# Kernel tuning notes

Hardware: AMD Instinct MI355X
Metric: run time of the kernel (lower is better)

## Reference

```python
import jax, jax.numpy as jnp
import numpy as np

Lx, Ly, D, P = 4, 5, 4, 2
DEPTH = 5
TAU = 0.1
N = Lx * Ly
B = 64


def setup_inputs() -> dict:
    key = jax.random.key(0)
    k1, k2, k3 = jax.random.split(key, 3)
    # PEPS site tensors: [Lx, Ly, phys, up, down, left, right]; boundary bonds sliced to dim 1 at use.
    peps = jax.random.normal(k1, (Lx, Ly, P, D, D, D, D), dtype=jnp.float32) * 0.5
    # Two-site Trotter gate: expm(-tau * h) for a random symmetric two-body term h (4x4).
    h = jax.random.normal(k2, (4, 4), dtype=jnp.float32)
    h = 0.5 * (h + h.T)
    w, v = jnp.linalg.eigh(h)
    gate = (v * jnp.exp(-TAU * w)) @ v.T  # [4,4]
    x = jax.random.randint(k3, (B, N), 0, 2, dtype=jnp.int32)
    return {"x": x, "peps": peps, "gate": gate}


def _slice_boundary(site, i, j):
    # site: [p, u, d, l, r]; open boundary -> bond dim 1 on lattice edges
    if i == 0:
        site = site[:, :1]
    if i == Lx - 1:
        site = site[:, :, :1]
    if j == 0:
        site = site[:, :, :, :1]
    if j == Ly - 1:
        site = site[..., :1]
    return site


def _peps_statevector(peps):
    # Exact contraction of the open-boundary PEPS to the full 2^N statevector.
    rows = []
    for i in range(Lx):
        T = jnp.ones((1, 1, 1, 1), dtype=peps.dtype)  # [Pphys, Uup, Ddown, l]
        for j in range(Ly):
            s = _slice_boundary(peps[i, j], i, j)
            T = jnp.einsum('PUDl,pudlr->PpUuDdr', T, s)
            Pn, p, U, u, Dn, d, r = T.shape
            T = T.reshape(Pn * p, U * u, Dn * d, r)
        rows.append(T[..., 0])  # [2^Ly, up_bonds, down_bonds]
    S = jnp.ones((1, 1), dtype=peps.dtype)  # [Pphys, down_bonds]
    for row in rows:
        S = jnp.einsum('PU,QUD->PQD', S, row)
        a, b, c = S.shape
        S = S.reshape(a * b, c)
    return S[:, 0]  # [2^N]


def _apply_gate(psi, g, a, b):
    # g: [2,2,2,2] = gate[o1,o2,i1,i2]; psi: (2,)*N
    out = jnp.tensordot(g, psi, axes=([2, 3], [a, b]))
    return jnp.moveaxis(out, (0, 1), (a, b))


def _bonds():
    horiz = [((i, j), (i, j + 1)) for i in range(Lx) for j in range(Ly - 1)]
    vert = [((i, j), (i + 1, j)) for i in range(Lx - 1) for j in range(Ly)]
    return horiz + vert


def reference(x, peps, gate):
    psi = _peps_statevector(peps).reshape((2,) * N)
    g = gate.reshape(2, 2, 2, 2)
    bonds = _bonds()
    for _ in range(DEPTH):
        for (i1, j1), (i2, j2) in bonds:
            psi = _apply_gate(psi, g, i1 * Ly + j1, i2 * Ly + j2)
    psi = psi.reshape(-1)
    pw = 2 ** jnp.arange(N - 1, -1, -1, dtype=jnp.int32)
    idx = (x * pw).sum(axis=1)
    return psi[idx]  # [B] amplitudes
```

## Files before the change

kernel.cpp:

```cpp
#include <hip/hip_runtime.h>


#define PAD(i) ((i) + (((i) >> 4) << 2))
#define PIDX(i,j,p,u,d,l,r) (((((((i)*5+(j))*2+(p))*4+(u))*4+(d))*4+(l))*4+(r))

static constexpr int COL0  = 0;
static constexpr int COL1  = 4096;
static constexpr int COL2  = COL1 + 1048576;
static constexpr int COL3  = COL2 + 1048576;
static constexpr int COL4  = COL3 + 1048576;
static constexpr int M01TO = COL4 + 4096;
static constexpr int M34TO = M01TO + 65536;
static constexpr int T12TO = M34TO + 65536;
static constexpr int PSIO  = T12TO + 1048576;

__global__ __launch_bounds__(256) void k_build_cols(const float* __restrict__ peps,
                                                    float* __restrict__ ws) {
  __shared__ float p01[4096], p23[4096];
  int bid = blockIdx.x, t = threadIdx.x;
  if (bid < 384) {
    int col = 1 + (bid >> 7);
    int part = bid & 127;
#pragma unroll
    for (int k = 0; k < 16; ++k) {
      int e = k * 256 + t;
      int r12 = e & 15, l12 = (e >> 4) & 15, d2 = (e >> 8) & 3, p = e >> 10;
      int l1 = l12 >> 2, l2 = l12 & 3, r1 = r12 >> 2, r2 = r12 & 3;
      float s01 = 0.f, s23 = 0.f;
#pragma unroll
      for (int d = 0; d < 4; ++d) {
        s01 += peps[PIDX(0, col, (p >> 1), 0, d, l1, r1)] *
               peps[PIDX(1, col, (p & 1), d, d2, l2, r2)];
        s23 += peps[PIDX(2, col, (p >> 1), d2, d, l1, r1)] *
               peps[PIDX(3, col, (p & 1), d, 0, l2, r2)];
      }
      p01[e] = s01;
      p23[e] = s23;
    }
    __syncthreads();
    const int coloffs[3] = {COL1, COL2, COL3};
    float* out = ws + coloffs[col - 1];
#pragma unroll
    for (int k = 0; k < 8; ++k) {
      int eq = part * 8192 + (k * 256 + t) * 4;
      int r34b = eq & 15;
      int r12 = (eq >> 4) & 15, l34 = (eq >> 8) & 15, l12 = (eq >> 12) & 15;
      int p = eq >> 16;
      int pa = p >> 2, pb = p & 3;
      float4 acc = {0.f, 0.f, 0.f, 0.f};
#pragma unroll
      for (int d2 = 0; d2 < 4; ++d2) {
        float a01 = p01[((((pa * 4 + d2) << 4) | l12) << 4) | r12];
        const float4 b4 =
            *(const float4*)&p23[((((pb * 4 + d2) << 4) | l34) << 4) | r34b];
        acc.x += a01 * b4.x;
        acc.y += a01 * b4.y;
        acc.z += a01 * b4.z;
        acc.w += a01 * b4.w;
      }
      *(float4*)&out[eq] = acc;
    }
  } else {
    int col = (bid == 384) ? 0 : 4;
    const int lsh = (col == 0) ? 0 : 2;
    const int rsh = (col == 4) ? 0 : 2;
    const int ldim = 1 << lsh, rdim = 1 << rsh;
    const int LLB = 2 * lsh, RRB = 2 * rsh;
    const int LL = 1 << LLB, RR = 1 << RRB;
    int n12 = (LL * RR) << 4;
    for (int e = t; e < n12; e += 256) {
      int r12 = e & (RR - 1);
      int l12 = (e >> RRB) & (LL - 1);
      int d2 = (e >> (RRB + LLB)) & 3;
      int p = e >> (RRB + LLB + 2);
      int l1 = l12 >> lsh, l2 = l12 & (ldim - 1);
      int r1 = r12 >> rsh, r2 = r12 & (rdim - 1);
      float s01 = 0.f, s23 = 0.f;
      for (int d = 0; d < 4; ++d) {
        s01 += peps[PIDX(0, col, (p >> 1), 0, d, l1, r1)] *
               peps[PIDX(1, col, (p & 1), d, d2, l2, r2)];
        s23 += peps[PIDX(2, col, (p >> 1), d2, d, l1, r1)] *
               peps[PIDX(3, col, (p & 1), d, 0, l2, r2)];
      }
      p01[e] = s01;
      p23[e] = s23;
    }
    __syncthreads();
    const int LB = 2 * LLB, RB = 2 * RRB;
    int total = 16 << (LB + RB);
    float* out = ws + ((col == 0) ? COL0 : COL4);
    for (int e = t; e < total; e += 256) {
      int r = e & ((1 << RB) - 1);
      int l = (e >> RB) & ((1 << LB) - 1);
      int p = e >> (RB + LB);
      int r34 = r & (RR - 1), r12 = r >> RRB;
      int l34 = l & (LL - 1), l12 = l >> LLB;
      int pa = p >> 2, pb = p & 3;
      float s = 0.f;
      for (int d2 = 0; d2 < 4; ++d2) {
        s += p01[((((pa * 4 + d2) << LLB) | l12) << RRB) | r12] *
             p23[((((pb * 4 + d2) << LLB) | l34) << RRB) | r34];
      }
      out[e] = s;
    }
  }
}

__global__ __launch_bounds__(256) void k_small(const float* __restrict__ ws,
                                               float* __restrict__ m01,
                                               float* __restrict__ m34t) {
  __shared__ float c3buf[4112], c4buf[4112];
  int t = threadIdx.x;
  if (blockIdx.x < 64) {
    int c1 = blockIdx.x >> 2, q = blockIdx.x & 3;
    int r2l = t & 63, c0g = t >> 6;
    int R2 = q * 64 + r2l;
    const float* col0 = ws + COL0;
    const float* col1 = ws + COL1;
    float a0 = 0.f, a1 = 0.f, a2 = 0.f, a3 = 0.f;
    for (int R1 = 0; R1 < 256; ++R1) {
      float bv = col1[(c1 * 256 + R1) * 256 + R2];
      a0 += col0[(c0g * 4 + 0) * 256 + R1] * bv;
      a1 += col0[(c0g * 4 + 1) * 256 + R1] * bv;
      a2 += col0[(c0g * 4 + 2) * 256 + R1] * bv;
      a3 += col0[(c0g * 4 + 3) * 256 + R1] * bv;
    }
    m01[((c0g * 4 + 0) * 16 + c1) * 256 + R2] = a0;
    m01[((c0g * 4 + 1) * 16 + c1) * 256 + R2] = a1;
    m01[((c0g * 4 + 2) * 16 + c1) * 256 + R2] = a2;
    m01[((c0g * 4 + 3) * 16 + c1) * 256 + R2] = a3;
  } else {
    int L3 = blockIdx.x - 64;
    const float* col3 = ws + COL3;
    const float* col4 = ws + COL4;
    for (int e = t; e < 4096; e += 256) {
      c4buf[(e >> 8) * 257 + (e & 255)] = col4[e];
      c3buf[(e >> 8) * 257 + (e & 255)] =
          col3[(e >> 8) * 65536 + L3 * 256 + (e & 255)];
    }
    __syncthreads();
    int c3 = t >> 4, c4 = t & 15;
    float acc = 0.f;
    for (int B = 0; B < 256; ++B)
      acc += c3buf[c3 * 257 + B] * c4buf[c4 * 257 + B];
    m34t[L3 * 256 + t] = acc;
  }
}

__global__ __launch_bounds__(256) void k_t012(const float* __restrict__ m01,
                                              const float* __restrict__ col2,
                                              float* __restrict__ t012) {
  __shared__ float A[4096];
  int t = threadIdx.x;
  int c2 = blockIdx.x & 15, tg = blockIdx.x >> 4;
#pragma unroll
  for (int k = 0; k < 4; ++k)
    *(float4*)&A[(k * 256 + t) * 4] =
        *(const float4*)&m01[tg * 4096 + (k * 256 + t) * 4];
  __syncthreads();
  float acc[16] = {};
  for (int R2 = 0; R2 < 256; R2 += 4) {
    float b0 = col2[c2 * 65536 + (R2 + 0) * 256 + t];
    float b1 = col2[c2 * 65536 + (R2 + 1) * 256 + t];
    float b2 = col2[c2 * 65536 + (R2 + 2) * 256 + t];
    float b3 = col2[c2 * 65536 + (R2 + 3) * 256 + t];
#pragma unroll
    for (int i = 0; i < 16; ++i) {
      float4 a4 = *(const float4*)&A[i * 256 + R2];
      acc[i] += a4.x * b0 + a4.y * b1 + a4.z * b2 + a4.w * b3;
    }
  }
#pragma unroll
  for (int i = 0; i < 16; ++i)
    t012[c2 * 65536 + (tg * 16 + i) * 256 + t] = acc[i];
}

__global__ __launch_bounds__(256) void k_psi0(const float* __restrict__ t012,
                                              const float* __restrict__ m34t,
                                              float* __restrict__ psi) {
  __shared__ float A[4096];
  int t = threadIdx.x;
  int tg = blockIdx.x;
#pragma unroll
  for (int i = 0; i < 16; ++i)
    A[i * 256 + t] = t012[i * 65536 + tg * 256 + t];
  __syncthreads();
  float acc[16] = {};
  for (int L3 = 0; L3 < 256; L3 += 4) {
    float b0 = m34t[(L3 + 0) * 256 + t];
    float b1 = m34t[(L3 + 1) * 256 + t];
    float b2 = m34t[(L3 + 2) * 256 + t];
    float b3 = m34t[(L3 + 3) * 256 + t];
#pragma unroll
    for (int i = 0; i < 16; ++i) {
      float4 a4 = *(const float4*)&A[i * 256 + L3];
      acc[i] += a4.x * b0 + a4.y * b1 + a4.z * b2 + a4.w * b3;
    }
  }
#pragma unroll
  for (int i = 0; i < 16; ++i)
    psi[(tg * 16 + i) * 256 + t] = acc[i];
}

template <int NB, int HI, int LO>
__device__ __forceinline__ void gate2(float* x, const float* __restrict__ g) {
  constexpr int H = 1 << HI, L = 1 << LO, N = 1 << NB;
#pragma unroll
  for (int o = 0; o < N; ++o) {
    if (o & (H | L)) continue;
    float v0 = x[o], v1 = x[o + L], v2 = x[o + H], v3 = x[o + H + L];
    x[o]         = g[0]  * v0 + g[1]  * v1 + g[2]  * v2 + g[3]  * v3;
    x[o + L]     = g[4]  * v0 + g[5]  * v1 + g[6]  * v2 + g[7]  * v3;
    x[o + H]     = g[8]  * v0 + g[9]  * v1 + g[10] * v2 + g[11] * v3;
    x[o + H + L] = g[12] * v0 + g[13] * v1 + g[14] * v2 + g[15] * v3;
  }
}

template <int ST>
__device__ __forceinline__ void vxf(float* s, const float* __restrict__ g, int b) {
  float x[16];
#pragma unroll
  for (int m = 0; m < 16; ++m) x[m] = s[PAD(b + m * ST)];
  gate2<4, 3, 2>(x, g);
  gate2<4, 2, 1>(x, g);
  gate2<4, 1, 0>(x, g);
#pragma unroll
  for (int m = 0; m < 16; ++m) s[PAD(b + m * ST)] = x[m];
}

template <int B2, int B1, int B0>
__device__ __forceinline__ void bondpair(float* s, const float* __restrict__ g,
                                         int t) {
  constexpr int MASK = (1 << B2) | (1 << B1) | (1 << B0);
#pragma unroll
  for (int k = 0; k < 2; ++k) {
    int gi = k * 256 + t;
    int b = 0, rem = gi;
#pragma unroll
    for (int p = 0; p < 12; ++p) {
      if (!((MASK >> p) & 1)) {
        b |= (rem & 1) << p;
        rem >>= 1;
      }
    }
    float x[8];
#pragma unroll
    for (int m = 0; m < 8; ++m) {
      int off = ((m >> 2) & 1) * (1 << B2) + ((m >> 1) & 1) * (1 << B1) +
                (m & 1) * (1 << B0);
      x[m] = s[PAD(b + off)];
    }
    gate2<3, 2, 1>(x, g);
    gate2<3, 1, 0>(x, g);
#pragma unroll
    for (int m = 0; m < 8; ++m) {
      int off = ((m >> 2) & 1) * (1 << B2) + ((m >> 1) & 1) * (1 << B1) +
                (m & 1) * (1 << B0);
      s[PAD(b + off)] = x[m];
    }
  }
}

template <bool FIRST>
__global__ __launch_bounds__(256) void k_P1(const float* __restrict__ src,
                                            float* __restrict__ dst,
                                            const float* __restrict__ gate) {
  __shared__ float s[5120];
  float g[16];
#pragma unroll
  for (int i = 0; i < 16; ++i) g[i] = gate[i];
  int t = threadIdx.x;
  int o;
  if (FIRST) {
    o = ((blockIdx.x & 7) << 5) | (blockIdx.x >> 3);
#pragma unroll
    for (int k = 0; k < 16; ++k) {
      int n = k * 256 + t;
      int addr = (n >> 8) * 65536 + ((n >> 4) & 15) * 4096 + (n & 15) * 256 +
                 (o >> 4) * 16 + (o & 15);
      s[PAD(n)] = src[addr];
    }
  } else {
    o = blockIdx.x;
#pragma unroll
    for (int i = 0; i < 4; ++i) {
      int f = (i * 256 + t) * 4;
      *(float4*)(s + PAD(f)) = *(const float4*)(src + o * 4096 + f);
    }
  }
  __syncthreads();
  bondpair<8, 4, 0>(s, g, t);
  __syncthreads();
  bondpair<9, 5, 1>(s, g, t);
  __syncthreads();
  bondpair<10, 6, 2>(s, g, t);
  __syncthreads();
  bondpair<11, 7, 3>(s, g, t);
  __syncthreads();
  vxf<256>(s, g, t);
  __syncthreads();
  vxf<16>(s, g, ((t >> 4) << 8) | (t & 15));
  __syncthreads();
#pragma unroll
  for (int i = 0; i < 4; ++i) {
    int f = (i * 256 + t) * 4;
    *(float4*)(dst + o * 4096 + f) = *(const float4*)(s + PAD(f));
  }
}

template <bool LAST>
__global__ __launch_bounds__(256) void k_P2(float* __restrict__ psi,
                                            const float* __restrict__ gate,
                                            const int* __restrict__ x,
                                            float* __restrict__ out) {
  __shared__ float s[5120];
  float g[16];
#pragma unroll
  for (int i = 0; i < 16; ++i) g[i] = gate[i];
  int t = threadIdx.x;
  int o = blockIdx.x;
#pragma unroll
  for (int i = 0; i < 4; ++i) {
    int f = (i * 256 + t) * 4;
    int addr = (f >> 8) * 65536 + ((f >> 4) & 15) * 4096 + o * 16 + (f & 15);
    *(float4*)(s + PAD(f)) = *(const float4*)(psi + addr);
  }
  __syncthreads();
  bondpair<0, 8, 4>(s, g, t);
  __syncthreads();
  bondpair<1, 9, 5>(s, g, t);
  __syncthreads();
  bondpair<2, 10, 6>(s, g, t);
  __syncthreads();
  bondpair<3, 11, 7>(s, g, t);
  __syncthreads();
  vxf<1>(s, g, t * 16);
  __syncthreads();
  vxf<256>(s, g, t);
  __syncthreads();
  vxf<16>(s, g, ((t >> 4) << 8) | (t & 15));
  __syncthreads();
  if (LAST) {
    if (t < 64) {
      int idx = 0;
#pragma unroll
      for (int q = 0; q < 20; ++q) {
        int i = q / 5, j = q % 5;
        int pos = (j == 0) ? (11 - i)
                 : (j == 1) ? (7 - i)
                 : (j == 2) ? (3 - i)
                 : (j == 3) ? (19 - i)
                            : (15 - i);
        idx |= x[t * 20 + q] << pos;
      }
      if (((idx >> 4) & 255) == o) {
        int local = ((idx >> 16) & 15) * 256 + ((idx >> 12) & 15) * 16 +
                    (idx & 15);
        out[t] = s[PAD(local)];
      }
    }
  } else {
#pragma unroll
    for (int i = 0; i < 4; ++i) {
      int f = (i * 256 + t) * 4;
      int addr = (f >> 8) * 65536 + ((f >> 4) & 15) * 4096 + o * 16 + (f & 15);
      *(float4*)(psi + addr) = *(const float4*)(s + PAD(f));
    }
  }
}

extern "C" void kernel_launch(void* const* d_in, const int* in_sizes, int n_in,
                              void* d_out, int out_size, void* d_ws, size_t ws_size,
                              hipStream_t stream) {
  const int* x = (const int*)d_in[0];
  const float* peps = (const float*)d_in[1];
  const float* gate = (const float*)d_in[2];
  float* ws = (float*)d_ws;
  float* psi_old = ws + PSIO;
  float* psi_new = ws + T12TO;
  float* out = (float*)d_out;

  k_build_cols<<<386, 256, 0, stream>>>(peps, ws);
  k_small<<<320, 256, 0, stream>>>(ws, ws + M01TO, ws + M34TO);
  k_t012<<<256, 256, 0, stream>>>(ws + M01TO, ws + COL2, ws + T12TO);
  k_psi0<<<256, 256, 0, stream>>>(ws + T12TO, ws + M34TO, psi_old);

  k_P1<true><<<256, 256, 0, stream>>>(psi_old, psi_new, gate);
  k_P2<false><<<256, 256, 0, stream>>>(psi_new, gate, x, out);
  for (int it = 1; it < 5; ++it) {
    k_P1<false><<<256, 256, 0, stream>>>(psi_new, psi_new, gate);
    if (it < 4)
      k_P2<false><<<256, 256, 0, stream>>>(psi_new, gate, x, out);
    else
      k_P2<true><<<256, 256, 0, stream>>>(psi_new, gate, x, out);
  }
}
```

Baseline: 221.6 us.

## Double gate-kernel threads to 512 and write psi0 directly in P1-friendly layout

The gate-application kernels now launch 512 threads per block, so each thread handles one bondpair group instead of two. This raises parallelism for the bondpair stages, while the vxf stages run on only half the threads. k_psi0 now transposes its output through shared memory into the layout P1 expects, which removes the scattered first-iteration load path and the separate FIRST variant. The costs are idle threads during vxf stages, more shared memory in k_psi0, and possible occupancy effects from the larger blocks.

```diff
diff --git a/kernel.cpp b/kernel.cpp
--- a/kernel.cpp
+++ b/kernel.cpp
@@ -179,6 +179,7 @@
                                               const float* __restrict__ m34t,
                                               float* __restrict__ psi) {
   __shared__ float A[4096];
+  __shared__ float S[4112];
   int t = threadIdx.x;
   int tg = blockIdx.x;
 #pragma unroll
@@ -198,8 +199,13 @@
     }
   }
 #pragma unroll
-  for (int i = 0; i < 16; ++i)
-    psi[(tg * 16 + i) * 256 + t] = acc[i];
+  for (int i = 0; i < 16; ++i) S[i * 257 + t] = acc[i];
+  __syncthreads();
+  int c3 = t >> 4, c2 = t & 15;
+  int base = c3 * 65536 + (tg >> 4) * 256 + (tg & 15) * 16 + c2;
+#pragma unroll
+  for (int v = 0; v < 16; ++v)
+    psi[base + v * 4096] = S[c2 * 257 + c3 * 16 + v];
 }
 
 template <int NB, int HI, int LO>
@@ -232,61 +238,43 @@
 __device__ __forceinline__ void bondpair(float* s, const float* __restrict__ g,
                                          int t) {
   constexpr int MASK = (1 << B2) | (1 << B1) | (1 << B0);
-#pragma unroll
-  for (int k = 0; k < 2; ++k) {
-    int gi = k * 256 + t;
-    int b = 0, rem = gi;
-#pragma unroll
-    for (int p = 0; p < 12; ++p) {
-      if (!((MASK >> p) & 1)) {
-        b |= (rem & 1) << p;
-        rem >>= 1;
-      }
-    }
-    float x[8];
-#pragma unroll
-    for (int m = 0; m < 8; ++m) {
-      int off = ((m >> 2) & 1) * (1 << B2) + ((m >> 1) & 1) * (1 << B1) +
-                (m & 1) * (1 << B0);
-      x[m] = s[PAD(b + off)];
-    }
-    gate2<3, 2, 1>(x, g);
-    gate2<3, 1, 0>(x, g);
-#pragma unroll
-    for (int m = 0; m < 8; ++m) {
-      int off = ((m >> 2) & 1) * (1 << B2) + ((m >> 1) & 1) * (1 << B1) +
-                (m & 1) * (1 << B0);
-      s[PAD(b + off)] = x[m];
-    }
-  }
-}
-
-template <bool FIRST>
-__global__ __launch_bounds__(256) void k_P1(const float* __restrict__ src,
-                                            float* __restrict__ dst,
+  int b = 0, rem = t;
+#pragma unroll
+  for (int p = 0; p < 12; ++p) {
+    if (!((MASK >> p) & 1)) {
+      b |= (rem & 1) << p;
+      rem >>= 1;
+    }
+  }
+  float x[8];
+#pragma unroll
+  for (int m = 0; m < 8; ++m) {
+    int off = ((m >> 2) & 1) * (1 << B2) + ((m >> 1) & 1) * (1 << B1) +
+              (m & 1) * (1 << B0);
+    x[m] = s[PAD(b + off)];
+  }
+  gate2<3, 2, 1>(x, g);
+  gate2<3, 1, 0>(x, g);
+#pragma unroll
+  for (int m = 0; m < 8; ++m) {
+    int off = ((m >> 2) & 1) * (1 << B2) + ((m >> 1) & 1) * (1 << B1) +
+              (m & 1) * (1 << B0);
+    s[PAD(b + off)] = x[m];
+  }
+}
+
+__global__ __launch_bounds__(512) void k_P1(float* __restrict__ psi,
                                             const float* __restrict__ gate) {
   __shared__ float s[5120];
   float g[16];
 #pragma unroll
   for (int i = 0; i < 16; ++i) g[i] = gate[i];
   int t = threadIdx.x;
-  int o;
-  if (FIRST) {
-    o = ((blockIdx.x & 7) << 5) | (blockIdx.x >> 3);
-#pragma unroll
-    for (int k = 0; k < 16; ++k) {
-      int n = k * 256 + t;
-      int addr = (n >> 8) * 65536 + ((n >> 4) & 15) * 4096 + (n & 15) * 256 +
-                 (o >> 4) * 16 + (o & 15);
-      s[PAD(n)] = src[addr];
-    }
-  } else {
-    o = blockIdx.x;
-#pragma unroll
-    for (int i = 0; i < 4; ++i) {
-      int f = (i * 256 + t) * 4;
-      *(float4*)(s + PAD(f)) = *(const float4*)(src + o * 4096 + f);
-    }
+  int o = blockIdx.x;
+#pragma unroll
+  for (int i = 0; i < 2; ++i) {
+    int f = (i * 512 + t) * 4;
+    *(float4*)(s + PAD(f)) = *(const float4*)(psi + o * 4096 + f);
   }
   __syncthreads();
   bondpair<8, 4, 0>(s, g, t);
@@ -297,19 +285,19 @@
   __syncthreads();
   bondpair<11, 7, 3>(s, g, t);
   __syncthreads();
-  vxf<256>(s, g, t);
-  __syncthreads();
-  vxf<16>(s, g, ((t >> 4) << 8) | (t & 15));
-  __syncthreads();
-#pragma unroll
-  for (int i = 0; i < 4; ++i) {
-    int f = (i * 256 + t) * 4;
-    *(float4*)(dst + o * 4096 + f) = *(const float4*)(s + PAD(f));
+  if (t < 256) vxf<256>(s, g, t);
+  __syncthreads();
+  if (t < 256) vxf<16>(s, g, ((t >> 4) << 8) | (t & 15));
+  __syncthreads();
+#pragma unroll
+  for (int i = 0; i < 2; ++i) {
+    int f = (i * 512 + t) * 4;
+    *(float4*)(psi + o * 4096 + f) = *(const float4*)(s + PAD(f));
   }
 }
 
 template <bool LAST>
-__global__ __launch_bounds__(256) void k_P2(float* __restrict__ psi,
+__global__ __launch_bounds__(512) void k_P2(float* __restrict__ psi,
                                             const float* __restrict__ gate,
                                             const int* __restrict__ x,
                                             float* __restrict__ out) {
@@ -320,8 +308,8 @@
   int t = threadIdx.x;
   int o = blockIdx.x;
 #pragma unroll
-  for (int i = 0; i < 4; ++i) {
-    int f = (i * 256 + t) * 4;
+  for (int i = 0; i < 2; ++i) {
+    int f = (i * 512 + t) * 4;
     int addr = (f >> 8) * 65536 + ((f >> 4) & 15) * 4096 + o * 16 + (f & 15);
     *(float4*)(s + PAD(f)) = *(const float4*)(psi + addr);
   }
@@ -334,11 +322,11 @@
   __syncthreads();
   bondpair<3, 11, 7>(s, g, t);
   __syncthreads();
-  vxf<1>(s, g, t * 16);
-  __syncthreads();
-  vxf<256>(s, g, t);
-  __syncthreads();
-  vxf<16>(s, g, ((t >> 4) << 8) | (t & 15));
+  if (t < 256) vxf<1>(s, g, t * 16);
+  __syncthreads();
+  if (t < 256) vxf<256>(s, g, t);
+  __syncthreads();
+  if (t < 256) vxf<16>(s, g, ((t >> 4) << 8) | (t & 15));
   __syncthreads();
   if (LAST) {
     if (t < 64) {
@@ -361,8 +349,8 @@
     }
   } else {
 #pragma unroll
-    for (int i = 0; i < 4; ++i) {
-      int f = (i * 256 + t) * 4;
+    for (int i = 0; i < 2; ++i) {
+      int f = (i * 512 + t) * 4;
       int addr = (f >> 8) * 65536 + ((f >> 4) & 15) * 4096 + o * 16 + (f & 15);
       *(float4*)(psi + addr) = *(const float4*)(s + PAD(f));
     }
@@ -376,22 +364,19 @@
   const float* peps = (const float*)d_in[1];
   const float* gate = (const float*)d_in[2];
   float* ws = (float*)d_ws;
-  float* psi_old = ws + PSIO;
-  float* psi_new = ws + T12TO;
+  float* psi = ws + PSIO;
   float* out = (float*)d_out;
 
   k_build_cols<<<386, 256, 0, stream>>>(peps, ws);
   k_small<<<320, 256, 0, stream>>>(ws, ws + M01TO, ws + M34TO);
   k_t012<<<256, 256, 0, stream>>>(ws + M01TO, ws + COL2, ws + T12TO);
-  k_psi0<<<256, 256, 0, stream>>>(ws + T12TO, ws + M34TO, psi_old);
-
-  k_P1<true><<<256, 256, 0, stream>>>(psi_old, psi_new, gate);
-  k_P2<false><<<256, 256, 0, stream>>>(psi_new, gate, x, out);
-  for (int it = 1; it < 5; ++it) {
-    k_P1<false><<<256, 256, 0, stream>>>(psi_new, psi_new, gate);
+  k_psi0<<<256, 256, 0, stream>>>(ws + T12TO, ws + M34TO, psi);
+
+  for (int it = 0; it < 5; ++it) {
+    k_P1<<<256, 512, 0, stream>>>(psi, gate);
     if (it < 4)
-      k_P2<false><<<256, 256, 0, stream>>>(psi_new, gate, x, out);
+      k_P2<false><<<256, 512, 0, stream>>>(psi, gate, x, out);
     else
-      k_P2<true><<<256, 256, 0, stream>>>(psi_new, gate, x, out);
-  }
-}
+      k_P2<true><<<256, 512, 0, stream>>>(psi, gate, x, out);
+  }
+}
```

Result: faster. 214.6 us (-3.2%).
